# Performance work log

Hardware: AMD Instinct MI355X
Metric: run time of the kernel (lower is better)

The kernel has to match this reference:

```python
import jax, jax.numpy as jnp
import numpy as np

N, S, C = 2048, 14, 30  # batch, grid, channels (B=2 boxes*5 + 20 classes)
L_COORD, L_NOOBJ = 5.0, 0.5


def setup_inputs() -> dict:
    key = jax.random.key(0)
    k1, k2, k3 = jax.random.split(key, 3)
    pred = jax.random.uniform(k1, (N, S, S, C), minval=0.05, maxval=1.0, dtype=jnp.float32)
    target = jax.random.uniform(k2, (N, S, S, C), minval=0.05, maxval=1.0, dtype=jnp.float32)
    conf = (jax.random.uniform(k3, (N, S, S)) > 0.7).astype(jnp.float32)
    target = target.at[..., 4].set(conf)
    return {"pred": pred, "target": target}


def _to_xyxy(b):
    # b[..., :2] = center (grid units, divided by 14), b[..., 2:4] = w,h (image units)
    xy = b[..., :2] / 14.0
    wh = b[..., 2:4]
    return jnp.concatenate([xy - 0.5 * wh, xy + 0.5 * wh], axis=-1)


def _yolo_loss(pred, target):
    n = pred.shape[0]
    coo = (target[..., 4] > 0).astype(pred.dtype)   # [N,S,S] object mask
    noo = 1.0 - coo                                  # no-object mask
    pb = pred[..., :10].reshape(pred.shape[:3] + (2, 5))    # [N,S,S,2,5]
    tb = target[..., :10].reshape(target.shape[:3] + (2, 5))

    # IoU of the 2 predicted boxes vs the FIRST target box of the cell
    p_xy = _to_xyxy(pb)              # [N,S,S,2,4]
    t_xy = _to_xyxy(tb[..., 0, :])   # [N,S,S,4]
    lt = jnp.maximum(p_xy[..., :2], t_xy[..., None, :2])
    rb = jnp.minimum(p_xy[..., 2:], t_xy[..., None, 2:])
    wh = jnp.clip(rb - lt, 0.0)
    inter = wh[..., 0] * wh[..., 1]                          # [N,S,S,2]
    a1 = (p_xy[..., 2] - p_xy[..., 0]) * (p_xy[..., 3] - p_xy[..., 1])
    a2 = ((t_xy[..., 2] - t_xy[..., 0]) * (t_xy[..., 3] - t_xy[..., 1]))[..., None]
    iou = inter / (a1 + a2 - inter)

    # responsible box = argmax IoU (selection only; IoU value never enters the
    # loss because the original writes max_iou into cols :4 but reads col 4=0)
    r = jnp.argmax(jax.lax.stop_gradient(iou), axis=-1)      # [N,S,S]
    idx = r[..., None, None]
    resp_p = jnp.take_along_axis(pb, idx, axis=3)[..., 0, :]      # [N,S,S,5]
    resp_t = jnp.take_along_axis(tb, idx, axis=3)[..., 0, :]
    nresp_p = jnp.take_along_axis(pb, 1 - idx, axis=3)[..., 0, :]

    cm = coo[..., None]
    loc = jnp.sum(cm * (resp_p[..., :2] - resp_t[..., :2]) ** 2) \
        + jnp.sum(cm * (jnp.sqrt(resp_p[..., 2:4]) - jnp.sqrt(resp_t[..., 2:4])) ** 2)
    contain = jnp.sum(coo * resp_p[..., 4] ** 2)       # target IoU col 4 is 0 in original
    not_contain = jnp.sum(coo * nresp_p[..., 4] ** 2)  # target conf zeroed in original
    noobj = jnp.sum(noo * ((pred[..., 4] - target[..., 4]) ** 2
                           + (pred[..., 9] - target[..., 9]) ** 2))
    cls = jnp.sum(cm * (pred[..., 10:] - target[..., 10:]) ** 2)
    return (L_COORD * loc + 2.0 * contain + not_contain + L_NOOBJ * noobj + cls) / n


def reference(pred, target):
    return _yolo_loss(pred, target)
```

## Files before the change

kernel.cpp:

```cpp
#include <hip/hip_runtime.h>


constexpr int N_IMG  = 2048;
constexpr int NC     = 30;
constexpr int CELLS  = N_IMG * 14 * 14;
constexpr int BLOCK  = 256;
constexpr int CPB    = 224;
constexpr int NCHUNK = 7;
constexpr int GRID   = 256;
constexpr float INV14 = 1.0f / 14.0f;

constexpr int NV  = CPB * NC / 4;
constexpr int REM = NV - (NV / BLOCK) * BLOCK;

__device__ __forceinline__ void gload16(const void* g, void* l) {
    __builtin_amdgcn_global_load_lds(
        (const __attribute__((address_space(1))) void*)g,
        (__attribute__((address_space(3))) void*)l, 16, 0, 0);
}

__device__ __forceinline__ float cell_loss(const float* __restrict__ cp,
                                           const float* __restrict__ ct)
{
    float pv[NC], tv[NC];
    const float2* p2 = reinterpret_cast<const float2*>(cp);
    const float2* t2 = reinterpret_cast<const float2*>(ct);
    #pragma unroll
    for (int i = 0; i < NC / 2; ++i) {
        float2 a = p2[i]; pv[2*i] = a.x; pv[2*i+1] = a.y;
        float2 b = t2[i]; tv[2*i] = b.x; tv[2*i+1] = b.y;
    }

    const float coo = (tv[4] > 0.0f) ? 1.0f : 0.0f;

    const float txc = tv[0] * INV14, tyc = tv[1] * INV14;
    const float tx1 = txc - 0.5f * tv[2], ty1 = tyc - 0.5f * tv[3];
    const float tx2 = txc + 0.5f * tv[2], ty2 = tyc + 0.5f * tv[3];
    const float t_area = (tx2 - tx1) * (ty2 - ty1);

    float i0, u0;
    {
        const float xc = pv[0] * INV14, yc = pv[1] * INV14;
        const float x1 = xc - 0.5f * pv[2], y1 = yc - 0.5f * pv[3];
        const float x2 = xc + 0.5f * pv[2], y2 = yc + 0.5f * pv[3];
        const float a1 = (x2 - x1) * (y2 - y1);
        const float wx = fmaxf(fminf(x2, tx2) - fmaxf(x1, tx1), 0.0f);
        const float wy = fmaxf(fminf(y2, ty2) - fmaxf(y1, ty1), 0.0f);
        i0 = wx * wy;
        u0 = a1 + t_area - i0;
    }
    float i1, u1;
    {
        const float xc = pv[5] * INV14, yc = pv[6] * INV14;
        const float x1 = xc - 0.5f * pv[7], y1 = yc - 0.5f * pv[8];
        const float x2 = xc + 0.5f * pv[7], y2 = yc + 0.5f * pv[8];
        const float a1 = (x2 - x1) * (y2 - y1);
        const float wx = fmaxf(fminf(x2, tx2) - fmaxf(x1, tx1), 0.0f);
        const float wy = fmaxf(fminf(y2, ty2) - fmaxf(y1, ty1), 0.0f);
        i1 = wx * wy;
        u1 = a1 + t_area - i1;
    }

    const bool sel = (i1 * u0) > (i0 * u1);
    const float rp0 = sel ? pv[5] : pv[0];
    const float rp1 = sel ? pv[6] : pv[1];
    const float rp2 = sel ? pv[7] : pv[2];
    const float rp3 = sel ? pv[8] : pv[3];
    const float rp4 = sel ? pv[9] : pv[4];
    const float rt0 = sel ? tv[5] : tv[0];
    const float rt1 = sel ? tv[6] : tv[1];
    const float rt2 = sel ? tv[7] : tv[2];
    const float rt3 = sel ? tv[8] : tv[3];
    const float nrp4 = sel ? pv[4] : pv[9];

    const float d0 = rp0 - rt0, d1 = rp1 - rt1;
    const float d2 = sqrtf(rp2) - sqrtf(rt2);
    const float d3 = sqrtf(rp3) - sqrtf(rt3);
    const float loc     = d0*d0 + d1*d1 + d2*d2 + d3*d3;
    const float contain = rp4 * rp4;
    const float notc    = nrp4 * nrp4;
    const float e4 = pv[4] - tv[4], e9 = pv[9] - tv[9];
    const float noobj = e4*e4 + e9*e9;
    float cls = 0.0f;
    #pragma unroll
    for (int c = 10; c < NC; ++c) { const float d = pv[c] - tv[c]; cls += d*d; }

    return coo * (5.0f * loc + 2.0f * contain + notc + cls)
         + (1.0f - coo) * (0.5f * noobj);
}

__global__ __launch_bounds__(BLOCK)
void yolo_main(const float* __restrict__ pred,
               const float* __restrict__ targ,
               float* __restrict__ partial)
{
    __shared__ float sp[2][CPB * NC];
    __shared__ float st[2][CPB * NC];

    const int tid = threadIdx.x;
    const int bid = blockIdx.x;

    auto stage = [&](int buf, int c) {
        const size_t fbase = (size_t)(bid * NCHUNK + c) * (size_t)(CPB * NC);
        const float4* gp = reinterpret_cast<const float4*>(pred + fbase);
        const float4* gt = reinterpret_cast<const float4*>(targ + fbase);
        float4* lp = reinterpret_cast<float4*>(sp[buf]);
        float4* lt = reinterpret_cast<float4*>(st[buf]);
        #pragma unroll
        for (int i = 0; i < NV / BLOCK; ++i)
            gload16(gp + i * BLOCK + tid, lp + i * BLOCK + tid);
        if (tid < REM)
            gload16(gp + (NV / BLOCK) * BLOCK + tid, lp + (NV / BLOCK) * BLOCK + tid);
        #pragma unroll
        for (int i = 0; i < NV / BLOCK; ++i)
            gload16(gt + i * BLOCK + tid, lt + i * BLOCK + tid);
        if (tid < REM)
            gload16(gt + (NV / BLOCK) * BLOCK + tid, lt + (NV / BLOCK) * BLOCK + tid);
    };

    stage(0, 0);
    __syncthreads();

    float acc = 0.0f;
    #pragma unroll
    for (int c = 0; c < NCHUNK; ++c) {
        const int buf = c & 1;
        if (c + 1 < NCHUNK) stage(buf ^ 1, c + 1);
        if (tid < CPB)
            acc += cell_loss(&sp[buf][tid * NC], &st[buf][tid * NC]);
        __syncthreads();
    }

    __shared__ float wsum[BLOCK / 64];
    #pragma unroll
    for (int o = 32; o > 0; o >>= 1) acc += __shfl_down(acc, o, 64);
    if ((tid & 63) == 0) wsum[tid >> 6] = acc;
    __syncthreads();
    if (tid == 0)
        partial[bid] = wsum[0] + wsum[1] + wsum[2] + wsum[3];
}

__global__ __launch_bounds__(64)
void yolo_final(const float* __restrict__ partial, float* __restrict__ out)
{
    const int tid = threadIdx.x;
    double s = 0.0;
    #pragma unroll
    for (int i = 0; i < GRID / 64; ++i) s += (double)partial[tid + i * 64];
    #pragma unroll
    for (int o = 32; o > 0; o >>= 1) s += __shfl_down(s, o, 64);
    if (tid == 0) out[0] = (float)(s / (double)N_IMG);
}

extern "C" void kernel_launch(void* const* d_in, const int* in_sizes, int n_in,
                              void* d_out, int out_size, void* d_ws, size_t ws_size,
                              hipStream_t stream)
{
    const float* pred = (const float*)d_in[0];
    const float* targ = (const float*)d_in[1];
    float* out        = (float*)d_out;
    float* partial    = (float*)d_ws;

    yolo_main<<<GRID, BLOCK, 0, stream>>>(pred, targ, partial);
    yolo_final<<<1, 64, 0, stream>>>(partial, out);
}
```

Before: 23.66 us.

## Halve cells per block, double grid, and merge pred/target staging loops

Cuts the cells per chunk to 112 and doubles the grid to 512 blocks, so more CUs receive work and each block's LDS footprint shrinks. The pred and target async LDS loads are merged into one combined index space so the rounds cover both arrays with a single remainder, which leaves fewer partially idle load rounds. The trade-off is that only 112 of 256 threads compute per chunk, so more lanes sit idle during the compute step, and there are twice as many partial sums to reduce.

Measured after the change: 23.05 us. -2.5%, faster.

```diff
diff --git a/kernel.cpp b/kernel.cpp
--- a/kernel.cpp
+++ b/kernel.cpp
@@ -5,13 +5,16 @@
 constexpr int NC     = 30;
 constexpr int CELLS  = N_IMG * 14 * 14;
 constexpr int BLOCK  = 256;
-constexpr int CPB    = 224;
+constexpr int CPB    = 112;
 constexpr int NCHUNK = 7;
-constexpr int GRID   = 256;
+constexpr int GRID   = 512;
 constexpr float INV14 = 1.0f / 14.0f;
 
-constexpr int NV  = CPB * NC / 4;
-constexpr int REM = NV - (NV / BLOCK) * BLOCK;
+constexpr int FPC   = CPB * NC;
+constexpr int NVA   = FPC / 4;
+constexpr int NVTOT = 2 * NVA;
+constexpr int ROUNDS = NVTOT / BLOCK;
+constexpr int REM    = NVTOT - ROUNDS * BLOCK;
 
 __device__ __forceinline__ void gload16(const void* g, void* l) {
     __builtin_amdgcn_global_load_lds(
@@ -94,28 +97,26 @@
                const float* __restrict__ targ,
                float* __restrict__ partial)
 {
-    __shared__ float sp[2][CPB * NC];
-    __shared__ float st[2][CPB * NC];
+    __shared__ float sbuf[2][2 * FPC];
 
     const int tid = threadIdx.x;
     const int bid = blockIdx.x;
 
     auto stage = [&](int buf, int c) {
-        const size_t fbase = (size_t)(bid * NCHUNK + c) * (size_t)(CPB * NC);
+        const size_t fbase = (size_t)(bid * NCHUNK + c) * (size_t)FPC;
         const float4* gp = reinterpret_cast<const float4*>(pred + fbase);
         const float4* gt = reinterpret_cast<const float4*>(targ + fbase);
-        float4* lp = reinterpret_cast<float4*>(sp[buf]);
-        float4* lt = reinterpret_cast<float4*>(st[buf]);
+        float4* lb = reinterpret_cast<float4*>(sbuf[buf]);
         #pragma unroll
-        for (int i = 0; i < NV / BLOCK; ++i)
-            gload16(gp + i * BLOCK + tid, lp + i * BLOCK + tid);
-        if (tid < REM)
-            gload16(gp + (NV / BLOCK) * BLOCK + tid, lp + (NV / BLOCK) * BLOCK + tid);
-        #pragma unroll
-        for (int i = 0; i < NV / BLOCK; ++i)
-            gload16(gt + i * BLOCK + tid, lt + i * BLOCK + tid);
-        if (tid < REM)
-            gload16(gt + (NV / BLOCK) * BLOCK + tid, lt + (NV / BLOCK) * BLOCK + tid);
+        for (int i = 0; i < ROUNDS; ++i) {
+            const int idx = i * BLOCK + tid;
+            const float4* src = (idx < NVA) ? (gp + idx) : (gt + (idx - NVA));
+            gload16(src, lb + idx);
+        }
+        if (tid < REM) {
+            const int idx = ROUNDS * BLOCK + tid;
+            gload16(gt + (idx - NVA), lb + idx);
+        }
     };
 
     stage(0, 0);
@@ -127,7 +128,7 @@
         const int buf = c & 1;
         if (c + 1 < NCHUNK) stage(buf ^ 1, c + 1);
         if (tid < CPB)
-            acc += cell_loss(&sp[buf][tid * NC], &st[buf][tid * NC]);
+            acc += cell_loss(&sbuf[buf][tid * NC], &sbuf[buf][FPC + tid * NC]);
         __syncthreads();
     }
 
```
